# Kernel optimization log

Hardware: AMD Instinct MI355X
Metric: run time of the kernel (lower is better)

## Reference

```python
import jax, jax.numpy as jnp
import numpy as np

C_S = 1024
H = 16
M = 1  # num_vector_messages
B, S = 2, 1024
SQRT3 = 3.0 ** 0.5
LN_EPS = 1e-5


def setup_inputs() -> dict:
    key = jax.random.key(0)
    ks = jax.random.split(key, 8)
    s = jax.random.normal(ks[0], (B, S, C_S), dtype=jnp.float32)
    # random proper-ish frames: orthonormalize random 3x3 via QR
    A = jax.random.normal(ks[1], (B, S, 3, 3), dtype=jnp.float32)
    rot, _ = jnp.linalg.qr(A)
    trans = jax.random.normal(ks[2], (B, S, 3), dtype=jnp.float32)
    affine_mask = jnp.ones((B, S), dtype=bool)
    sequence_id = jax.random.randint(ks[3], (B, S), 0, 4, dtype=jnp.int32)
    chain_id = jax.random.randint(ks[4], (B, S), 0, 4, dtype=jnp.int32)
    dim_proj = 4 * H * 3 + H * 3 * M
    ln_w = jnp.ones((C_S,), dtype=jnp.float32)
    w_proj = jax.random.normal(ks[5], (dim_proj, C_S), dtype=jnp.float32) / np.sqrt(C_S)
    w_out = jax.random.normal(ks[6], (C_S, H * 3 * M), dtype=jnp.float32) / np.sqrt(H * 3 * M)
    dist_scale = jnp.zeros((H,), dtype=jnp.float32)
    rot_scale = jnp.zeros((H,), dtype=jnp.float32)
    return {"s": s, "rot": rot, "trans": trans, "ln_w": ln_w, "w_proj": w_proj,
            "w_out": w_out, "dist_scale": dist_scale, "rot_scale": rot_scale,
            "affine_mask": affine_mask, "sequence_id": sequence_id, "chain_id": chain_id}


def reference(s, rot, trans, ln_w, w_proj, w_out, dist_scale, rot_scale,
              affine_mask, sequence_id, chain_id):
    b, n, c = s.shape
    h, m = H, M
    NEG = jnp.finfo(s.dtype).min
    # attention bias: 1.0 for same-sequence pairs, -inf for invalid frames / cross-chain
    seq_eq = (sequence_id[:, :, None] == sequence_id[:, None, :]).astype(s.dtype)
    bias = seq_eq[:, None]  # [b,1,s,s]
    bias = jnp.where(affine_mask[:, None, None, :], bias, NEG)
    chain_diff = chain_id[:, :, None] != chain_id[:, None, :]
    bias = jnp.where(chain_diff[:, None], NEG, bias)
    # LayerNorm (no bias)
    mu = jnp.mean(s, axis=-1, keepdims=True)
    var = jnp.var(s, axis=-1, keepdims=True)
    ns = (s - mu) / jnp.sqrt(var + LN_EPS) * ln_w
    p = jnp.einsum('bsc,dc->bsd', ns, w_proj)
    n_rot = h * 2 * 3 + h * 3 * m
    vec_rot = p[..., :n_rot].reshape(b, n, 2 * h + h * m, 3)
    vec_dist = p[..., n_rot:].reshape(b, n, 2 * h, 3)
    # rotate into global frame; dist vectors also translated
    rot_vecs = jnp.einsum('bsij,bshj->bshi', rot, vec_rot)
    q_rot, k_rot, value = rot_vecs[:, :, :h], rot_vecs[:, :, h:2 * h], rot_vecs[:, :, 2 * h:]
    dist_vecs = jnp.einsum('bsij,bshj->bshi', rot, vec_dist) + trans[:, :, None, :]
    q_dist, k_dist = dist_vecs[:, :, :h], dist_vecs[:, :, h:]
    # distance term [b,h,q,k]
    qd = q_dist.transpose(0, 2, 1, 3)  # b h s 3
    kd = k_dist.transpose(0, 2, 1, 3)
    diff = qd[:, :, :, None, :] - kd[:, :, None, :, :]
    distance_term = jnp.sqrt(jnp.sum(diff * diff, axis=-1)) / SQRT3
    rotation_term = jnp.einsum('bqhd,bkhd->bhqk', q_rot, k_rot) / SQRT3
    dw = jax.nn.softplus(dist_scale)[None, :, None, None]
    rw = jax.nn.softplus(rot_scale)[None, :, None, None]
    attn = rotation_term * rw - distance_term * dw + bias
    attn = jax.nn.softmax(attn, axis=-1)
    # value: b s (h m) 3 -> b h s (m 3)
    v = value.reshape(b, n, h, m, 3).transpose(0, 2, 1, 3, 4).reshape(b, h, n, m * 3)
    out = jnp.einsum('bhqk,bhkd->bhqd', attn, v)
    out = out.reshape(b, h, n, m, 3).transpose(0, 2, 1, 3, 4).reshape(b, n, h * m, 3)
    out = jnp.einsum('bsji,bshj->bshi', rot, out)  # inverse rotation R^T
    out = out.reshape(b, n, h * m * 3)
    out = jnp.where(affine_mask[..., None], out, 0.0)
    return jnp.einsum('bsd,cd->bsc', out, w_out)
```

## Files before the change

kernel.cpp:

```cpp
#include <hip/hip_runtime.h>
#include <math.h>

#define NB 2
#define NS 1024
#define NC 1024
#define NH 16
#define DIMP 240
#define KSPLIT 8

constexpr float INV_SQRT3 = 0.57735026919f;

__global__ __launch_bounds__(256) void ln_kernel(const float* __restrict__ s,
                                                 const float* __restrict__ lnw,
                                                 float* __restrict__ ns) {
    int row = blockIdx.x;
    int tid = threadIdx.x;
    const float4* sp = (const float4*)(s + (size_t)row * NC);
    float4 v = sp[tid];
    float sum = v.x + v.y + v.z + v.w;
    float sq  = v.x*v.x + v.y*v.y + v.z*v.z + v.w*v.w;
    #pragma unroll
    for (int off = 32; off; off >>= 1) {
        sum += __shfl_down(sum, off);
        sq  += __shfl_down(sq, off);
    }
    __shared__ float s1[4], s2[4];
    int wave = tid >> 6;
    if ((tid & 63) == 0) { s1[wave] = sum; s2[wave] = sq; }
    __syncthreads();
    float tot   = s1[0] + s1[1] + s1[2] + s1[3];
    float totsq = s2[0] + s2[1] + s2[2] + s2[3];
    float mu  = tot * (1.0f / NC);
    float var = totsq * (1.0f / NC) - mu * mu;
    float rstd = rsqrtf(var + 1e-5f);
    float4 w = ((const float4*)lnw)[tid];
    float4 o;
    o.x = (v.x - mu) * rstd * w.x;
    o.y = (v.y - mu) * rstd * w.y;
    o.z = (v.z - mu) * rstd * w.z;
    o.w = (v.w - mu) * rstd * w.w;
    ((float4*)(ns + (size_t)row * NC))[tid] = o;
}

__global__ __launch_bounds__(256) void wtrans_kernel(const float* __restrict__ wp,
                                                     float* __restrict__ wt) {
    int k0 = (blockIdx.x & 15) * 64;
    int d0 = (blockIdx.x >> 4) * 60;
    __shared__ float T[64][61];
    int tid = threadIdx.x;
    #pragma unroll
    for (int i = 0; i < 15; i++) {
        int idx = i * 256 + tid;
        int dd = idx >> 6, kk = idx & 63;
        T[kk][dd] = wp[(size_t)(d0 + dd) * NC + k0 + kk];
    }
    __syncthreads();
    #pragma unroll
    for (int i = 0; i < 15; i++) {
        int idx = i * 256 + tid;
        int kk = idx / 60, dd = idx % 60;
        wt[(size_t)(k0 + kk) * DIMP + d0 + dd] = T[kk][dd];
    }
}

__global__ __launch_bounds__(256) void proj_kernel(const float* __restrict__ ns,
                                                   const float* __restrict__ wt,
                                                   float* __restrict__ pp,
                                                   int use_atomic) {
    int tid = threadIdx.x;
    int wave = tid >> 6, lane = tid & 63;
    int row0 = blockIdx.x * 32;
    int ky = blockIdx.y;
    int k0 = ky * 128;

    __shared__ float A[32][128];
    #pragma unroll
    for (int i = 0; i < 4; i++) {
        int idx = tid + i * 256;
        int r = idx >> 5, c4 = idx & 31;
        *(float4*)&A[r][c4 * 4] = *(const float4*)(ns + (size_t)(row0 + r) * NC + k0 + c4 * 4);
    }
    __syncthreads();

    int wr0 = wave * 8;
    int c0 = lane * 4;
    bool active = c0 < DIMP;
    int c0m = active ? c0 : (DIMP - 4);
    const float* wb = wt + (size_t)k0 * DIMP + c0m;

    float acc[8][4];
    #pragma unroll
    for (int r = 0; r < 8; r++)
        #pragma unroll
        for (int c = 0; c < 4; c++) acc[r][c] = 0.0f;

    float4 wa[4], wx[4];
    #pragma unroll
    for (int j = 0; j < 4; j++) wa[j] = *(const float4*)(wb + (size_t)j * DIMP);

    for (int g = 0; g < 32; g += 2) {
        #pragma unroll
        for (int j = 0; j < 4; j++)
            wx[j] = *(const float4*)(wb + (size_t)((g + 1) * 4 + j) * DIMP);
        #pragma unroll
        for (int r = 0; r < 8; r++) {
            float4 a4 = *(const float4*)&A[wr0 + r][g * 4];
            #pragma unroll
            for (int c = 0; c < 4; c++) {
                float* ac = &acc[r][c];
                *ac = fmaf(a4.x, ((const float*)&wa[0])[c], *ac);
                *ac = fmaf(a4.y, ((const float*)&wa[1])[c], *ac);
                *ac = fmaf(a4.z, ((const float*)&wa[2])[c], *ac);
                *ac = fmaf(a4.w, ((const float*)&wa[3])[c], *ac);
            }
        }
        int kn2 = (g + 2 < 32) ? (g + 2) * 4 : 0;
        #pragma unroll
        for (int j = 0; j < 4; j++)
            wa[j] = *(const float4*)(wb + (size_t)(kn2 + j) * DIMP);
        #pragma unroll
        for (int r = 0; r < 8; r++) {
            float4 a4 = *(const float4*)&A[wr0 + r][(g + 1) * 4];
            #pragma unroll
            for (int c = 0; c < 4; c++) {
                float* ac = &acc[r][c];
                *ac = fmaf(a4.x, ((const float*)&wx[0])[c], *ac);
                *ac = fmaf(a4.y, ((const float*)&wx[1])[c], *ac);
                *ac = fmaf(a4.z, ((const float*)&wx[2])[c], *ac);
                *ac = fmaf(a4.w, ((const float*)&wx[3])[c], *ac);
            }
        }
    }
    if (active) {
        if (use_atomic) {
            #pragma unroll
            for (int r = 0; r < 8; r++)
                #pragma unroll
                for (int c = 0; c < 4; c++)
                    atomicAdd(&pp[(size_t)(row0 + wr0 + r) * DIMP + c0 + c], acc[r][c]);
        } else {
            float* dst = pp + (size_t)ky * (NB * NS * DIMP);
            #pragma unroll
            for (int r = 0; r < 8; r++)
                *(float4*)(dst + (size_t)(row0 + wr0 + r) * DIMP + c0) =
                    make_float4(acc[r][0], acc[r][1], acc[r][2], acc[r][3]);
        }
    }
}

__global__ __launch_bounds__(256) void reduce_kernel(float4* __restrict__ pp) {
    int i = blockIdx.x * 256 + threadIdx.x;
    const int stride = NB * NS * DIMP / 4;
    float4 s = pp[i];
    #pragma unroll
    for (int ky = 1; ky < KSPLIT; ky++) {
        float4 t = pp[i + (size_t)ky * stride];
        s.x += t.x; s.y += t.y; s.z += t.z; s.w += t.w;
    }
    pp[i] = s;
}

__global__ __launch_bounds__(256) void build_kernel(const float* __restrict__ p,
                                                    const float* __restrict__ rot,
                                                    const float* __restrict__ trans,
                                                    const float* __restrict__ dist_scale,
                                                    const float* __restrict__ rot_scale,
                                                    const int* __restrict__ seq,
                                                    const int* __restrict__ chain,
                                                    const int* __restrict__ amask,
                                                    float4* __restrict__ qr, float4* __restrict__ kr,
                                                    float4* __restrict__ vv, float4* __restrict__ qd,
                                                    float4* __restrict__ kd,
                                                    int* __restrict__ meta) {
    int gid = blockIdx.x * 256 + threadIdx.x;
    if (gid >= NB * NS * 80) return;
    int j  = gid % 80;
    int bs = gid / 80;
    int b  = bs >> 10;
    int si = bs & 1023;
    if (j == 0)
        meta[bs] = (amask[bs] << 16) | (chain[bs] << 8) | seq[bs];
    const float* R  = rot + (size_t)bs * 9;
    const float* pr = p + (size_t)bs * DIMP;
    int off = (j < 48) ? 3 * j : 144 + 3 * (j - 48);
    float vx = pr[off], vy = pr[off + 1], vz = pr[off + 2];
    float ox = R[0] * vx + R[1] * vy + R[2] * vz;
    float oy = R[3] * vx + R[4] * vy + R[5] * vz;
    float oz = R[6] * vx + R[7] * vy + R[8] * vz;
    if (j >= 48) {
        ox += trans[(size_t)bs * 3 + 0];
        oy += trans[(size_t)bs * 3 + 1];
        oz += trans[(size_t)bs * 3 + 2];
    }
    float scale = 1.0f;
    if (j < 16)                   scale = log1pf(__expf(rot_scale[j]))  * INV_SQRT3;
    else if (j >= 48)             scale = log1pf(__expf(dist_scale[(j - 48) & 15])) * INV_SQRT3;
    ox *= scale; oy *= scale; oz *= scale;
    float4 o4 = make_float4(ox, oy, oz, 0.0f);
    if (j < 16)       qr[(size_t)(b * NH + j)        * NS + si] = o4;
    else if (j < 32)  kr[(size_t)(b * NH + (j - 16)) * NS + si] = o4;
    else if (j < 48)  vv[(size_t)(b * NH + (j - 32)) * NS + si] = o4;
    else if (j < 64)  qd[(size_t)(b * NH + (j - 48)) * NS + si] = o4;
    else              kd[(size_t)(b * NH + (j - 64)) * NS + si] = o4;
}

__global__ __launch_bounds__(256) void attn_kernel(
    const float4* __restrict__ qr, const float4* __restrict__ kr,
    const float4* __restrict__ qd, const float4* __restrict__ kd,
    const float4* __restrict__ vv,
    const float* __restrict__ rot,
    const int* __restrict__ meta,
    float* __restrict__ small) {
    int wid  = blockIdx.x * 4 + (threadIdx.x >> 6);
    int lane = threadIdx.x & 63;
    int qg = wid & 255;
    int h  = (wid >> 8) & 15;
    int b  = wid >> 12;
    int base = (b * NH + h) * NS;
    int q0 = qg * 4;

    float qrx[4], qry[4], qrz[4], qdx[4], qdy[4], qdz[4];
    int vq[4], sq[4], amq[4];
    #pragma unroll
    for (int t = 0; t < 4; t++) {
        float4 a = qr[base + q0 + t];
        float4 d = qd[base + q0 + t];
        qrx[t] = a.x; qry[t] = a.y; qrz[t] = a.z;
        qdx[t] = d.x; qdy[t] = d.y; qdz[t] = d.z;
        int mq = meta[b * NS + q0 + t];
        vq[t]  = 0x100 | ((mq >> 8) & 255);
        sq[t]  = mq & 255;
        amq[t] = mq >> 16;
    }
    float l[4] = {0, 0, 0, 0}, ax[4] = {0, 0, 0, 0}, ay[4] = {0, 0, 0, 0}, az[4] = {0, 0, 0, 0};

    for (int k = lane; k < NS; k += 64) {
        float4 kv = kr[base + k];
        float4 dv = kd[base + k];
        float4 vk = vv[base + k];
        int mk = meta[b * NS + k];
        int mkhi = mk >> 8, mklo = mk & 255;
        #pragma unroll
        for (int t = 0; t < 4; t++) {
            float rt = fmaf(qrx[t], kv.x, fmaf(qry[t], kv.y, qrz[t] * kv.z));
            float dx = qdx[t] - dv.x, dy = qdy[t] - dv.y, dz = qdz[t] - dv.z;
            float d2 = fmaf(dx, dx, fmaf(dy, dy, dz * dz));
            float arg = rt - sqrtf(d2) + ((mklo == sq[t]) ? -15.0f : -16.0f);
            float pw = (mkhi == vq[t]) ? __expf(arg) : 0.0f;
            l[t] += pw;
            ax[t] = fmaf(pw, vk.x, ax[t]);
            ay[t] = fmaf(pw, vk.y, ay[t]);
            az[t] = fmaf(pw, vk.z, az[t]);
        }
    }
    #pragma unroll
    for (int t = 0; t < 4; t++) {
        #pragma unroll
        for (int off = 32; off; off >>= 1) {
            l[t]  += __shfl_xor(l[t], off);
            ax[t] += __shfl_xor(ax[t], off);
            ay[t] += __shfl_xor(ay[t], off);
            az[t] += __shfl_xor(az[t], off);
        }
    }
    if (lane == 0) {
        #pragma unroll
        for (int t = 0; t < 4; t++) {
            int q = q0 + t;
            float inv = 1.0f / l[t];
            float ox = ax[t] * inv, oy = ay[t] * inv, oz = az[t] * inv;
            const float* R = rot + (size_t)(b * NS + q) * 9;
            float wx = R[0] * ox + R[3] * oy + R[6] * oz;
            float wy = R[1] * ox + R[4] * oy + R[7] * oz;
            float wz = R[2] * ox + R[5] * oy + R[8] * oz;
            if (!amq[t]) { wx = 0; wy = 0; wz = 0; }
            float* o = small + (size_t)(b * NS + q) * 48 + h * 3;
            o[0] = wx; o[1] = wy; o[2] = wz;
        }
    }
}

__global__ __launch_bounds__(256) void outgemm_kernel(const float* __restrict__ small,
                                                      const float* __restrict__ wout,
                                                      float* __restrict__ out) {
    int c  = blockIdx.y * 256 + threadIdx.x;
    int r0 = blockIdx.x * 16;
    __shared__ float sm[16][48];
    for (int i = threadIdx.x; i < 16 * 48; i += 256)
        sm[i / 48][i % 48] = small[(size_t)(r0 + i / 48) * 48 + i % 48];
    __syncthreads();
    float w[48];
    #pragma unroll
    for (int d = 0; d < 48; d += 4) {
        float4 t = *(const float4*)(wout + (size_t)c * 48 + d);
        w[d] = t.x; w[d + 1] = t.y; w[d + 2] = t.z; w[d + 3] = t.w;
    }
    #pragma unroll 4
    for (int r = 0; r < 16; r++) {
        float acc = 0.0f;
        #pragma unroll
        for (int d = 0; d < 48; d++) acc = fmaf(w[d], sm[r][d], acc);
        out[(size_t)(r0 + r) * NC + c] = acc;
    }
}

extern "C" void kernel_launch(void* const* d_in, const int* in_sizes, int n_in,
                              void* d_out, int out_size, void* d_ws, size_t ws_size,
                              hipStream_t stream) {
    const float* s     = (const float*)d_in[0];
    const float* rot   = (const float*)d_in[1];
    const float* trans = (const float*)d_in[2];
    const float* lnw   = (const float*)d_in[3];
    const float* wproj = (const float*)d_in[4];
    const float* wout  = (const float*)d_in[5];
    const float* dsc   = (const float*)d_in[6];
    const float* rsc   = (const float*)d_in[7];
    const int* amask   = (const int*)d_in[8];
    const int* seq     = (const int*)d_in[9];
    const int* chain   = (const int*)d_in[10];
    float* out = (float*)d_out;

    float* ns = (float*)d_ws;
    float4* qr = (float4*)(ns + (size_t)NB * NS * NC);
    float4* kr = qr + (size_t)NB * NH * NS;
    float4* vv = kr + (size_t)NB * NH * NS;
    float4* qd = vv + (size_t)NB * NH * NS;
    float4* kd = qd + (size_t)NB * NH * NS;
    float* small = (float*)(kd + (size_t)NB * NH * NS);
    int* meta = (int*)(small + (size_t)NB * NS * 48);
    float* pp = (float*)(meta + NB * NS);
    float* p  = pp;
    float* wt = (float*)qr;

    size_t need = ((char*)(pp + (size_t)KSPLIT * NB * NS * DIMP)) - (char*)d_ws;
    int use_atomic = (ws_size < need) ? 1 : 0;

    ln_kernel<<<NB * NS, 256, 0, stream>>>(s, lnw, ns);
    wtrans_kernel<<<64, 256, 0, stream>>>(wproj, wt);
    if (use_atomic) {
        hipMemsetAsync(p, 0, (size_t)NB * NS * DIMP * sizeof(float), stream);
        proj_kernel<<<dim3(64, KSPLIT), 256, 0, stream>>>(ns, wt, p, 1);
    } else {
        proj_kernel<<<dim3(64, KSPLIT), 256, 0, stream>>>(ns, wt, pp, 0);
        reduce_kernel<<<NB * NS * DIMP / 4 / 256, 256, 0, stream>>>((float4*)pp);
    }
    build_kernel<<<(NB * NS * 80 + 255) / 256, 256, 0, stream>>>(p, rot, trans, dsc, rsc,
                                                                 seq, chain, amask,
                                                                 qr, kr, vv, qd, kd, meta);
    attn_kernel<<<NB * NH * NS / 16, 256, 0, stream>>>(qr, kr, qd, kd, vv, rot, meta, small);
    outgemm_kernel<<<dim3(NB * NS / 16, 4), 256, 0, stream>>>(small, wout, out);
}
```

Measured before the change: 161.3 us.

## Fuse LN with weight transpose, fold split-K reduce into build, pack key data

LayerNorm and the weight transpose now run in one launch. The split-K factor for the projection GEMM doubles to raise parallelism, and the separate reduce kernel is removed by summing the partials inside build_kernel. Key-side rotation, distance and value vectors are interleaved into one packed array, with chain/mask and sequence id carried in the .w lanes. The chain and mask test becomes a large negative arithmetic penalty instead of an integer compare. In exchange, build_kernel reads more partial sums, and the float-encoded chain penalty changes masking semantics slightly: masked keys are no longer exact zeros.

After: 156.1 us. 1.03x faster.

```diff
diff --git a/kernel.cpp b/kernel.cpp
--- a/kernel.cpp
+++ b/kernel.cpp
@@ -6,60 +6,62 @@
 #define NC 1024
 #define NH 16
 #define DIMP 240
-#define KSPLIT 8
+#define KSPLIT 16
 
 constexpr float INV_SQRT3 = 0.57735026919f;
 
-__global__ __launch_bounds__(256) void ln_kernel(const float* __restrict__ s,
-                                                 const float* __restrict__ lnw,
-                                                 float* __restrict__ ns) {
-    int row = blockIdx.x;
+__global__ __launch_bounds__(256) void pre_kernel(const float* __restrict__ s,
+                                                  const float* __restrict__ lnw,
+                                                  float* __restrict__ ns,
+                                                  const float* __restrict__ wp,
+                                                  float* __restrict__ wt) {
+    __shared__ float sh[64 * 61];
     int tid = threadIdx.x;
-    const float4* sp = (const float4*)(s + (size_t)row * NC);
-    float4 v = sp[tid];
-    float sum = v.x + v.y + v.z + v.w;
-    float sq  = v.x*v.x + v.y*v.y + v.z*v.z + v.w*v.w;
-    #pragma unroll
-    for (int off = 32; off; off >>= 1) {
-        sum += __shfl_down(sum, off);
-        sq  += __shfl_down(sq, off);
-    }
-    __shared__ float s1[4], s2[4];
-    int wave = tid >> 6;
-    if ((tid & 63) == 0) { s1[wave] = sum; s2[wave] = sq; }
-    __syncthreads();
-    float tot   = s1[0] + s1[1] + s1[2] + s1[3];
-    float totsq = s2[0] + s2[1] + s2[2] + s2[3];
-    float mu  = tot * (1.0f / NC);
-    float var = totsq * (1.0f / NC) - mu * mu;
-    float rstd = rsqrtf(var + 1e-5f);
-    float4 w = ((const float4*)lnw)[tid];
-    float4 o;
-    o.x = (v.x - mu) * rstd * w.x;
-    o.y = (v.y - mu) * rstd * w.y;
-    o.z = (v.z - mu) * rstd * w.z;
-    o.w = (v.w - mu) * rstd * w.w;
-    ((float4*)(ns + (size_t)row * NC))[tid] = o;
-}
-
-__global__ __launch_bounds__(256) void wtrans_kernel(const float* __restrict__ wp,
-                                                     float* __restrict__ wt) {
-    int k0 = (blockIdx.x & 15) * 64;
-    int d0 = (blockIdx.x >> 4) * 60;
-    __shared__ float T[64][61];
-    int tid = threadIdx.x;
-    #pragma unroll
-    for (int i = 0; i < 15; i++) {
-        int idx = i * 256 + tid;
-        int dd = idx >> 6, kk = idx & 63;
-        T[kk][dd] = wp[(size_t)(d0 + dd) * NC + k0 + kk];
-    }
-    __syncthreads();
-    #pragma unroll
-    for (int i = 0; i < 15; i++) {
-        int idx = i * 256 + tid;
-        int kk = idx / 60, dd = idx % 60;
-        wt[(size_t)(k0 + kk) * DIMP + d0 + dd] = T[kk][dd];
+    if (blockIdx.x < NB * NS) {
+        int row = blockIdx.x;
+        const float4* sp = (const float4*)(s + (size_t)row * NC);
+        float4 v = sp[tid];
+        float sum = v.x + v.y + v.z + v.w;
+        float sq  = v.x*v.x + v.y*v.y + v.z*v.z + v.w*v.w;
+        #pragma unroll
+        for (int off = 32; off; off >>= 1) {
+            sum += __shfl_down(sum, off);
+            sq  += __shfl_down(sq, off);
+        }
+        float* s1 = sh; float* s2 = sh + 4;
+        int wave = tid >> 6;
+        if ((tid & 63) == 0) { s1[wave] = sum; s2[wave] = sq; }
+        __syncthreads();
+        float tot   = s1[0] + s1[1] + s1[2] + s1[3];
+        float totsq = s2[0] + s2[1] + s2[2] + s2[3];
+        float mu  = tot * (1.0f / NC);
+        float var = totsq * (1.0f / NC) - mu * mu;
+        float rstd = rsqrtf(var + 1e-5f);
+        float4 w = ((const float4*)lnw)[tid];
+        float4 o;
+        o.x = (v.x - mu) * rstd * w.x;
+        o.y = (v.y - mu) * rstd * w.y;
+        o.z = (v.z - mu) * rstd * w.z;
+        o.w = (v.w - mu) * rstd * w.w;
+        ((float4*)(ns + (size_t)row * NC))[tid] = o;
+    } else {
+        int bx = blockIdx.x - NB * NS;
+        int k0 = (bx & 15) * 64;
+        int d0 = (bx >> 4) * 60;
+        float (*T)[61] = (float (*)[61])sh;
+        #pragma unroll
+        for (int i = 0; i < 15; i++) {
+            int idx = i * 256 + tid;
+            int dd = idx >> 6, kk = idx & 63;
+            T[kk][dd] = wp[(size_t)(d0 + dd) * NC + k0 + kk];
+        }
+        __syncthreads();
+        #pragma unroll
+        for (int i = 0; i < 15; i++) {
+            int idx = i * 256 + tid;
+            int kk = idx / 60, dd = idx % 60;
+            wt[(size_t)(k0 + kk) * DIMP + d0 + dd] = T[kk][dd];
+        }
     }
 }
 
@@ -71,13 +73,13 @@
     int wave = tid >> 6, lane = tid & 63;
     int row0 = blockIdx.x * 32;
     int ky = blockIdx.y;
-    int k0 = ky * 128;
-
-    __shared__ float A[32][128];
-    #pragma unroll
-    for (int i = 0; i < 4; i++) {
+    int k0 = ky * 64;
+
+    __shared__ float A[32][64];
+    #pragma unroll
+    for (int i = 0; i < 2; i++) {
         int idx = tid + i * 256;
-        int r = idx >> 5, c4 = idx & 31;
+        int r = idx >> 4, c4 = idx & 15;
         *(float4*)&A[r][c4 * 4] = *(const float4*)(ns + (size_t)(row0 + r) * NC + k0 + c4 * 4);
     }
     __syncthreads();
@@ -98,7 +100,7 @@
     #pragma unroll
     for (int j = 0; j < 4; j++) wa[j] = *(const float4*)(wb + (size_t)j * DIMP);
 
-    for (int g = 0; g < 32; g += 2) {
+    for (int g = 0; g < 16; g += 2) {
         #pragma unroll
         for (int j = 0; j < 4; j++)
             wx[j] = *(const float4*)(wb + (size_t)((g + 1) * 4 + j) * DIMP);
@@ -114,7 +116,7 @@
                 *ac = fmaf(a4.w, ((const float*)&wa[3])[c], *ac);
             }
         }
-        int kn2 = (g + 2 < 32) ? (g + 2) * 4 : 0;
+        int kn2 = (g + 2 < 16) ? (g + 2) * 4 : 0;
         #pragma unroll
         for (int j = 0; j < 4; j++)
             wa[j] = *(const float4*)(wb + (size_t)(kn2 + j) * DIMP);
@@ -148,19 +150,7 @@
     }
 }
 
-__global__ __launch_bounds__(256) void reduce_kernel(float4* __restrict__ pp) {
-    int i = blockIdx.x * 256 + threadIdx.x;
-    const int stride = NB * NS * DIMP / 4;
-    float4 s = pp[i];
-    #pragma unroll
-    for (int ky = 1; ky < KSPLIT; ky++) {
-        float4 t = pp[i + (size_t)ky * stride];
-        s.x += t.x; s.y += t.y; s.z += t.z; s.w += t.w;
-    }
-    pp[i] = s;
-}
-
-__global__ __launch_bounds__(256) void build_kernel(const float* __restrict__ p,
+__global__ __launch_bounds__(256) void build_kernel(const float* __restrict__ pp, int nred,
                                                     const float* __restrict__ rot,
                                                     const float* __restrict__ trans,
                                                     const float* __restrict__ dist_scale,
@@ -168,22 +158,22 @@
                                                     const int* __restrict__ seq,
                                                     const int* __restrict__ chain,
                                                     const int* __restrict__ amask,
-                                                    float4* __restrict__ qr, float4* __restrict__ kr,
-                                                    float4* __restrict__ vv, float4* __restrict__ qd,
-                                                    float4* __restrict__ kd,
-                                                    int* __restrict__ meta) {
+                                                    float4* __restrict__ qrb,
+                                                    float4* __restrict__ qdb,
+                                                    float4* __restrict__ kp) {
     int gid = blockIdx.x * 256 + threadIdx.x;
     if (gid >= NB * NS * 80) return;
     int j  = gid % 80;
     int bs = gid / 80;
     int b  = bs >> 10;
     int si = bs & 1023;
-    if (j == 0)
-        meta[bs] = (amask[bs] << 16) | (chain[bs] << 8) | seq[bs];
-    const float* R  = rot + (size_t)bs * 9;
-    const float* pr = p + (size_t)bs * DIMP;
     int off = (j < 48) ? 3 * j : 144 + 3 * (j - 48);
-    float vx = pr[off], vy = pr[off + 1], vz = pr[off + 2];
+    float vx = 0.0f, vy = 0.0f, vz = 0.0f;
+    for (int ky = 0; ky < nred; ky++) {
+        const float* pr = pp + (size_t)ky * (NB * NS * DIMP) + (size_t)bs * DIMP + off;
+        vx += pr[0]; vy += pr[1]; vz += pr[2];
+    }
+    const float* R = rot + (size_t)bs * 9;
     float ox = R[0] * vx + R[1] * vy + R[2] * vz;
     float oy = R[3] * vx + R[4] * vy + R[5] * vz;
     float oz = R[6] * vx + R[7] * vy + R[8] * vz;
@@ -192,24 +182,32 @@
         oy += trans[(size_t)bs * 3 + 1];
         oz += trans[(size_t)bs * 3 + 2];
     }
-    float scale = 1.0f;
-    if (j < 16)                   scale = log1pf(__expf(rot_scale[j]))  * INV_SQRT3;
-    else if (j >= 48)             scale = log1pf(__expf(dist_scale[(j - 48) & 15])) * INV_SQRT3;
-    ox *= scale; oy *= scale; oz *= scale;
-    float4 o4 = make_float4(ox, oy, oz, 0.0f);
-    if (j < 16)       qr[(size_t)(b * NH + j)        * NS + si] = o4;
-    else if (j < 32)  kr[(size_t)(b * NH + (j - 16)) * NS + si] = o4;
-    else if (j < 48)  vv[(size_t)(b * NH + (j - 32)) * NS + si] = o4;
-    else if (j < 64)  qd[(size_t)(b * NH + (j - 48)) * NS + si] = o4;
-    else              kd[(size_t)(b * NH + (j - 64)) * NS + si] = o4;
+    if (j < 16) {
+        float sc = log1pf(__expf(rot_scale[j])) * INV_SQRT3;
+        qrb[(size_t)(b * NH + j) * NS + si] = make_float4(ox * sc, oy * sc, oz * sc, 0.0f);
+    } else if (j < 32) {
+        int h = j - 16;
+        float ck = (float)chain[bs] + 1000.0f * (float)(1 - amask[bs]);
+        kp[((size_t)(b * NH + h) * NS + si) * 3 + 0] = make_float4(ox, oy, oz, ck);
+    } else if (j < 48) {
+        int h = j - 32;
+        kp[((size_t)(b * NH + h) * NS + si) * 3 + 2] = make_float4(ox, oy, oz, 0.0f);
+    } else if (j < 64) {
+        int h = j - 48;
+        float sc = log1pf(__expf(dist_scale[h])) * INV_SQRT3;
+        qdb[(size_t)(b * NH + h) * NS + si] = make_float4(ox * sc, oy * sc, oz * sc, 0.0f);
+    } else {
+        int h = j - 64;
+        float sc = log1pf(__expf(dist_scale[h])) * INV_SQRT3;
+        kp[((size_t)(b * NH + h) * NS + si) * 3 + 1] =
+            make_float4(ox * sc, oy * sc, oz * sc, (float)seq[bs]);
+    }
 }
 
 __global__ __launch_bounds__(256) void attn_kernel(
-    const float4* __restrict__ qr, const float4* __restrict__ kr,
-    const float4* __restrict__ qd, const float4* __restrict__ kd,
-    const float4* __restrict__ vv,
+    const float4* __restrict__ qrb, const float4* __restrict__ qdb,
+    const float4* __restrict__ kp,
     const float* __restrict__ rot,
-    const int* __restrict__ meta,
     float* __restrict__ small) {
     int wid  = blockIdx.x * 4 + (threadIdx.x >> 6);
     int lane = threadIdx.x & 63;
@@ -218,39 +216,38 @@
     int b  = wid >> 12;
     int base = (b * NH + h) * NS;
     int q0 = qg * 4;
-
-    float qrx[4], qry[4], qrz[4], qdx[4], qdy[4], qdz[4];
-    int vq[4], sq[4], amq[4];
+    const float4* kb = kp + (size_t)base * 3;
+
+    float qrx[4], qry[4], qrz[4], qdx[4], qdy[4], qdz[4], cq[4], sq[4];
     #pragma unroll
     for (int t = 0; t < 4; t++) {
-        float4 a = qr[base + q0 + t];
-        float4 d = qd[base + q0 + t];
+        float4 a = qrb[base + q0 + t];
+        float4 d = qdb[base + q0 + t];
         qrx[t] = a.x; qry[t] = a.y; qrz[t] = a.z;
         qdx[t] = d.x; qdy[t] = d.y; qdz[t] = d.z;
-        int mq = meta[b * NS + q0 + t];
-        vq[t]  = 0x100 | ((mq >> 8) & 255);
-        sq[t]  = mq & 255;
-        amq[t] = mq >> 16;
+        cq[t] = kb[(size_t)(q0 + t) * 3 + 0].w;
+        sq[t] = kb[(size_t)(q0 + t) * 3 + 1].w;
     }
     float l[4] = {0, 0, 0, 0}, ax[4] = {0, 0, 0, 0}, ay[4] = {0, 0, 0, 0}, az[4] = {0, 0, 0, 0};
 
     for (int k = lane; k < NS; k += 64) {
-        float4 kv = kr[base + k];
-        float4 dv = kd[base + k];
-        float4 vk = vv[base + k];
-        int mk = meta[b * NS + k];
-        int mkhi = mk >> 8, mklo = mk & 255;
+        float4 f0 = kb[(size_t)k * 3 + 0];
+        float4 f1 = kb[(size_t)k * 3 + 1];
+        float4 f2 = kb[(size_t)k * 3 + 2];
         #pragma unroll
         for (int t = 0; t < 4; t++) {
-            float rt = fmaf(qrx[t], kv.x, fmaf(qry[t], kv.y, qrz[t] * kv.z));
-            float dx = qdx[t] - dv.x, dy = qdy[t] - dv.y, dz = qdz[t] - dv.z;
+            float rt = fmaf(qrx[t], f0.x, fmaf(qry[t], f0.y, qrz[t] * f0.z));
+            float dx = qdx[t] - f1.x, dy = qdy[t] - f1.y, dz = qdz[t] - f1.z;
             float d2 = fmaf(dx, dx, fmaf(dy, dy, dz * dz));
-            float arg = rt - sqrtf(d2) + ((mklo == sq[t]) ? -15.0f : -16.0f);
-            float pw = (mkhi == vq[t]) ? __expf(arg) : 0.0f;
+            float dist = sqrtf(d2);
+            float dc = f0.w - cq[t];
+            float arg = fmaf(-100.0f, fabsf(dc), rt - dist) +
+                        ((f1.w == sq[t]) ? -15.0f : -16.0f);
+            float pw = __expf(arg);
             l[t] += pw;
-            ax[t] = fmaf(pw, vk.x, ax[t]);
-            ay[t] = fmaf(pw, vk.y, ay[t]);
-            az[t] = fmaf(pw, vk.z, az[t]);
+            ax[t] = fmaf(pw, f2.x, ax[t]);
+            ay[t] = fmaf(pw, f2.y, ay[t]);
+            az[t] = fmaf(pw, f2.z, az[t]);
         }
     }
     #pragma unroll
@@ -273,7 +270,7 @@
             float wx = R[0] * ox + R[3] * oy + R[6] * oz;
             float wy = R[1] * ox + R[4] * oy + R[7] * oz;
             float wz = R[2] * ox + R[5] * oy + R[8] * oz;
-            if (!amq[t]) { wx = 0; wy = 0; wz = 0; }
+            if (cq[t] >= 500.0f) { wx = 0; wy = 0; wz = 0; }
             float* o = small + (size_t)(b * NS + q) * 48 + h * 3;
             o[0] = wx; o[1] = wy; o[2] = wz;
         }
@@ -321,32 +318,27 @@
     float* out = (float*)d_out;
 
     float* ns = (float*)d_ws;
-    float4* qr = (float4*)(ns + (size_t)NB * NS * NC);
-    float4* kr = qr + (size_t)NB * NH * NS;
-    float4* vv = kr + (size_t)NB * NH * NS;
-    float4* qd = vv + (size_t)NB * NH * NS;
-    float4* kd = qd + (size_t)NB * NH * NS;
-    float* small = (float*)(kd + (size_t)NB * NH * NS);
-    int* meta = (int*)(small + (size_t)NB * NS * 48);
-    float* pp = (float*)(meta + NB * NS);
-    float* p  = pp;
-    float* wt = (float*)qr;
+    float4* qrb = (float4*)(ns + (size_t)NB * NS * NC);
+    float4* qdb = qrb + (size_t)NB * NH * NS;
+    float4* kpk = qdb + (size_t)NB * NH * NS;
+    float* small = (float*)(kpk + (size_t)3 * NB * NH * NS);
+    float* pp = small + (size_t)NB * NS * 48;
+    float* wt = (float*)qrb;
 
     size_t need = ((char*)(pp + (size_t)KSPLIT * NB * NS * DIMP)) - (char*)d_ws;
     int use_atomic = (ws_size < need) ? 1 : 0;
 
-    ln_kernel<<<NB * NS, 256, 0, stream>>>(s, lnw, ns);
-    wtrans_kernel<<<64, 256, 0, stream>>>(wproj, wt);
+    pre_kernel<<<NB * NS + 64, 256, 0, stream>>>(s, lnw, ns, wproj, wt);
     if (use_atomic) {
-        hipMemsetAsync(p, 0, (size_t)NB * NS * DIMP * sizeof(float), stream);
-        proj_kernel<<<dim3(64, KSPLIT), 256, 0, stream>>>(ns, wt, p, 1);
+        hipMemsetAsync(pp, 0, (size_t)NB * NS * DIMP * sizeof(float), stream);
+        proj_kernel<<<dim3(64, KSPLIT), 256, 0, stream>>>(ns, wt, pp, 1);
+        build_kernel<<<(NB * NS * 80 + 255) / 256, 256, 0, stream>>>(pp, 1, rot, trans, dsc, rsc,
+                                                                     seq, chain, amask, qrb, qdb, kpk);
     } else {
         proj_kernel<<<dim3(64, KSPLIT), 256, 0, stream>>>(ns, wt, pp, 0);
-        reduce_kernel<<<NB * NS * DIMP / 4 / 256, 256, 0, stream>>>((float4*)pp);
-    }
-    build_kernel<<<(NB * NS * 80 + 255) / 256, 256, 0, stream>>>(p, rot, trans, dsc, rsc,
-                                                                 seq, chain, amask,
-                                                                 qr, kr, vv, qd, kd, meta);
-    attn_kernel<<<NB * NH * NS / 16, 256, 0, stream>>>(qr, kr, qd, kd, vv, rot, meta, small);
+        build_kernel<<<(NB * NS * 80 + 255) / 256, 256, 0, stream>>>(pp, KSPLIT, rot, trans, dsc, rsc,
+                                                                     seq, chain, amask, qrb, qdb, kpk);
+    }
+    attn_kernel<<<NB * NH * NS / 16, 256, 0, stream>>>(qrb, qdb, kpk, rot, small);
     outgemm_kernel<<<dim3(NB * NS / 16, 4), 256, 0, stream>>>(small, wout, out);
 }
```
